# Kernel tuning notes

Hardware: AMD Instinct MI355X
Metric: run time of the kernel (lower is better)

The kernel has to match this reference:

```python
import jax, jax.numpy as jnp
import numpy as np

GAMMA = 0.1
B, C, H, W = 8, 64, 64, 64
CINT = C // 8


def setup_inputs() -> dict:
    key = jax.random.key(0)
    ks = jax.random.split(key, 5)
    x = jax.random.normal(ks[0], (B, C, H, W), dtype=jnp.float32)
    Wq = jax.random.normal(ks[1], (CINT, C), dtype=jnp.float32) * 0.05
    Wk = jax.random.normal(ks[2], (CINT, C), dtype=jnp.float32) * 0.05
    Wv = jax.random.normal(ks[3], (CINT, C), dtype=jnp.float32) * 0.05
    Wout = jax.random.normal(ks[4], (C, CINT), dtype=jnp.float32) * 0.05
    return {"x": x, "Wq": Wq, "Wk": Wk, "Wv": Wv, "Wout": Wout}


def reference(x, Wq, Wk, Wv, Wout):
    b, c, h, w = x.shape
    n = h * w
    cint = Wq.shape[0]
    xf = x.reshape(b, c, n)                               # [B,C,N]
    q = jnp.einsum('ic,bcn->bin', Wq, xf)                 # [B,Cint,N]
    k = jnp.einsum('ic,bcn->bin', Wk, xf)
    v = jnp.einsum('ic,bcn->bin', Wv, xf)
    # scores[b, n, m] = q[b,:,n] . k[b,:,m]; softmax over dim=1 (the n axis)
    scores = jnp.einsum('bin,bim->bnm', q, k) / jnp.sqrt(jnp.asarray(cint, x.dtype))
    att = jax.nn.softmax(scores, axis=1)                  # [B,N,N], softmax over rows
    att_out = jnp.einsum('bin,bnm->bim', v, att)          # [B,Cint,N]
    out = jnp.einsum('ci,bim->bcm', Wout, att_out)        # [B,C,N]
    return x + out.reshape(b, c, h, w) * GAMMA
```

## Files before the change

### kernel.cpp

```cpp
#include <hip/hip_runtime.h>
#include <math.h>

#define BB 8
#define CC 64
#define NN 4096
#define CI 8
#define GAMMA 0.1f
#define SCALE (1.44269504088896f * 0.35355339059327f)
#define NSPLIT 8

typedef float v4f  __attribute__((ext_vector_type(4)));
typedef float v16f __attribute__((ext_vector_type(16)));
typedef __bf16 bf16x8 __attribute__((ext_vector_type(8)));
typedef __bf16 bf16x4 __attribute__((ext_vector_type(4)));
typedef unsigned int u32x2 __attribute__((ext_vector_type(2)));

__device__ __forceinline__ float fast_exp2(float x) {
    return __builtin_amdgcn_exp2f(x);
}

__device__ __forceinline__ unsigned int cvt_pk_bf16(float lo, float hi) {
    unsigned int r;
    asm("v_cvt_pk_bf16_f32 %0, %1, %2" : "=v"(r) : "v"(lo), "v"(hi));
    return r;
}

__global__ __launch_bounds__(256) void qkv_kernel(
        const float* __restrict__ x,
        const float* __restrict__ Wq, const float* __restrict__ Wk,
        const float* __restrict__ Wv,
        __bf16* __restrict__ qbh, __bf16* __restrict__ kbh,
        __bf16* __restrict__ vbh, float* __restrict__ attab) {
    __shared__ float sw[3 * CI * CC];
    __shared__ unsigned short sq[32 * 8];
    __shared__ unsigned short sk[32 * 8];
    const int t = threadIdx.x;
    const int i  = t >> 5;
    const int nl = t & 31;
    const int b  = blockIdx.y;
    const int n0 = blockIdx.x * 32;

    for (int idx = t; idx < CI * CC; idx += 256) {
        sw[idx]                = Wq[idx];
        sw[CI * CC + idx]      = Wk[idx] * SCALE;
        sw[2 * CI * CC + idx]  = Wv[idx];
    }
    int lin = (blockIdx.y * (NN / 32) + blockIdx.x) * 256 + t;
    for (int idx = lin; idx < BB * 9 * NN; idx += BB * NN * CI) attab[idx] = 0.f;
    __syncthreads();

    const int n = n0 + nl;
    const float* xp = x + ((size_t)b * CC) * NN + n;
    const v4f* wq4 = (const v4f*)(sw + i * CC);
    const v4f* wk4 = (const v4f*)(sw + CI * CC + i * CC);
    const v4f* wv4 = (const v4f*)(sw + 2 * CI * CC + i * CC);
    float qa = 0.f, ka = 0.f, va = 0.f;
#pragma unroll 4
    for (int c4 = 0; c4 < CC / 4; ++c4) {
        v4f wq = wq4[c4], wk = wk4[c4], wv = wv4[c4];
        float x0 = xp[(size_t)(c4 * 4 + 0) * NN];
        float x1 = xp[(size_t)(c4 * 4 + 1) * NN];
        float x2 = xp[(size_t)(c4 * 4 + 2) * NN];
        float x3 = xp[(size_t)(c4 * 4 + 3) * NN];
        qa = fmaf(wq.x, x0, qa); ka = fmaf(wk.x, x0, ka); va = fmaf(wv.x, x0, va);
        qa = fmaf(wq.y, x1, qa); ka = fmaf(wk.y, x1, ka); va = fmaf(wv.y, x1, va);
        qa = fmaf(wq.z, x2, qa); ka = fmaf(wk.z, x2, ka); va = fmaf(wv.z, x2, va);
        qa = fmaf(wq.w, x3, qa); ka = fmaf(wk.w, x3, ka); va = fmaf(wv.w, x3, va);
    }
    __bf16 vb = (__bf16)va;
    vbh[((size_t)b * CI + i) * NN + n] = vb;
    __bf16 qb = (__bf16)qa, kb2 = (__bf16)ka;
    sq[nl * 8 + i] = *(unsigned short*)&qb;
    sk[nl * 8 + i] = *(unsigned short*)&kb2;
    __syncthreads();
    if (t < 32) {
        *(uint4*)(qbh + ((size_t)b * NN + n0 + t) * 8) = *(const uint4*)(sq + t * 8);
        *(uint4*)(kbh + ((size_t)b * NN + n0 + t) * 8) = *(const uint4*)(sk + t * 8);
    }
}

__global__ __launch_bounds__(256) void att_kernel(
        const __bf16* __restrict__ qbh, const __bf16* __restrict__ kbh,
        const __bf16* __restrict__ vbh, float* __restrict__ attab) {
    const int t = threadIdx.x;
    const int w    = t >> 6;
    const int l    = t & 63;
    const int ln   = l & 31;
    const int hi   = l >> 5;
    const int b  = blockIdx.z;
    const int m0 = blockIdx.x * 128 + w * 32;
    const int nbase = blockIdx.y * (NN / NSPLIT);
    const int NCH = (NN / NSPLIT) / 32;

    bf16x8 zero8, ones8;
#pragma unroll
    for (int z = 0; z < 8; ++z) { zero8[z] = (__bf16)0.0f; ones8[z] = (__bf16)1.0f; }

    bf16x8 kfragB = hi ? zero8
                       : *(const bf16x8*)(kbh + ((size_t)b * NN + m0 + ln) * 8);

    const __bf16* qrow = qbh + (size_t)b * NN * 8;
    const __bf16* vrow = vbh + ((size_t)b * CI + (ln & 7)) * NN;
    const bool v_live = (ln < 8);
    const bool v_ones = (ln == 8);

    v16f acc = {0.f,0.f,0.f,0.f,0.f,0.f,0.f,0.f,0.f,0.f,0.f,0.f,0.f,0.f,0.f,0.f};

    for (int ch = 0; ch < NCH; ++ch) {
        const int nc = nbase + ch * 32;
        bf16x8 qfrag = hi ? zero8
                          : *(const bf16x8*)(qrow + (size_t)(nc + ln) * 8);
        bf16x8 va0 = v_live ? *(const bf16x8*)(vrow + nc + hi * 8)
                            : (v_ones ? ones8 : zero8);
        bf16x8 va1 = v_live ? *(const bf16x8*)(vrow + nc + 16 + hi * 8)
                            : (v_ones ? ones8 : zero8);

        v16f S = __builtin_amdgcn_mfma_f32_32x32x16_bf16(
            qfrag, kfragB,
            (v16f){0.f,0.f,0.f,0.f,0.f,0.f,0.f,0.f,0.f,0.f,0.f,0.f,0.f,0.f,0.f,0.f},
            0, 0, 0);

        unsigned int pk0 = cvt_pk_bf16(fast_exp2(S[0]),  fast_exp2(S[1]));
        unsigned int pk1 = cvt_pk_bf16(fast_exp2(S[2]),  fast_exp2(S[3]));
        unsigned int pk2 = cvt_pk_bf16(fast_exp2(S[4]),  fast_exp2(S[5]));
        unsigned int pk3 = cvt_pk_bf16(fast_exp2(S[6]),  fast_exp2(S[7]));
        unsigned int pk4 = cvt_pk_bf16(fast_exp2(S[8]),  fast_exp2(S[9]));
        unsigned int pk5 = cvt_pk_bf16(fast_exp2(S[10]), fast_exp2(S[11]));
        unsigned int pk6 = cvt_pk_bf16(fast_exp2(S[12]), fast_exp2(S[13]));
        unsigned int pk7 = cvt_pk_bf16(fast_exp2(S[14]), fast_exp2(S[15]));

        u32x2 r02 = __builtin_amdgcn_permlane32_swap(pk0, pk2, false, false);
        u32x2 r13 = __builtin_amdgcn_permlane32_swap(pk1, pk3, false, false);
        u32x2 r46 = __builtin_amdgcn_permlane32_swap(pk4, pk6, false, false);
        u32x2 r57 = __builtin_amdgcn_permlane32_swap(pk5, pk7, false, false);

        union { unsigned int u[4]; bf16x8 f; } e0f, e1f;
        e0f.u[0] = r02[0]; e0f.u[1] = r13[0]; e0f.u[2] = r02[1]; e0f.u[3] = r13[1];
        e1f.u[0] = r46[0]; e1f.u[1] = r57[0]; e1f.u[2] = r46[1]; e1f.u[3] = r57[1];

        acc = __builtin_amdgcn_mfma_f32_32x32x16_bf16(va0, e0f.f, acc, 0, 0, 0);
        acc = __builtin_amdgcn_mfma_f32_32x32x16_bf16(va1, e1f.f, acc, 0, 0, 0);
    }

    float* ap = attab + (size_t)b * 9 * NN + m0 + ln;
#pragma unroll
    for (int r = 0; r < 16; ++r) {
        int io = (r & 3) + 8 * (r >> 2) + 4 * hi;
        if (io < 9) atomicAdd(ap + (size_t)io * NN, acc[r]);
    }
}

__global__ __launch_bounds__(256) void out_kernel(
        const float* __restrict__ x, const float* __restrict__ Wout,
        const float* __restrict__ attab, float* __restrict__ out) {
    const int t = threadIdx.x;
    const int c = blockIdx.y;
    const int b = blockIdx.z;
    const int m = (blockIdx.x * 256 + t) * 4;
    const float* ap = attab + (size_t)b * 9 * NN + m;
    v4f sum = *(const v4f*)(ap + (size_t)8 * NN);
    v4f s = {0.f, 0.f, 0.f, 0.f};
#pragma unroll
    for (int i = 0; i < CI; ++i) {
        float wgt = Wout[c * CI + i];
        v4f a = *(const v4f*)(ap + (size_t)i * NN);
        s.x = fmaf(wgt, a.x, s.x);
        s.y = fmaf(wgt, a.y, s.y);
        s.z = fmaf(wgt, a.z, s.z);
        s.w = fmaf(wgt, a.w, s.w);
    }
    size_t o = ((size_t)b * CC + c) * NN + m;
    v4f xv = *(const v4f*)(x + o);
    v4f r;
    r.x = xv.x + GAMMA * (s.x / sum.x);
    r.y = xv.y + GAMMA * (s.y / sum.y);
    r.z = xv.z + GAMMA * (s.z / sum.z);
    r.w = xv.w + GAMMA * (s.w / sum.w);
    *(v4f*)(out + o) = r;
}

extern "C" void kernel_launch(void* const* d_in, const int* in_sizes, int n_in,
                              void* d_out, int out_size, void* d_ws, size_t ws_size,
                              hipStream_t stream) {
    const float* x    = (const float*)d_in[0];
    const float* Wq   = (const float*)d_in[1];
    const float* Wk   = (const float*)d_in[2];
    const float* Wv   = (const float*)d_in[3];
    const float* Wout = (const float*)d_in[4];
    float* out = (float*)d_out;

    __bf16* qbh = (__bf16*)d_ws;
    __bf16* kbh = qbh + (size_t)BB * NN * 8;
    __bf16* vbh = kbh + (size_t)BB * NN * 8;
    float* attab = (float*)(vbh + (size_t)BB * NN * 8);

    qkv_kernel<<<dim3(NN / 32, BB), 256, 0, stream>>>(x, Wq, Wk, Wv, qbh, kbh, vbh, attab);
    att_kernel<<<dim3(NN / 128, NSPLIT, BB), 256, 0, stream>>>(qbh, kbh, vbh, attab);
    out_kernel<<<dim3(NN / 1024, CC, BB), 256, 0, stream>>>(x, Wout, attab, out);
}
```

Measured before the change: 108.3 us.

## Pad V to 32 rows, prefetch next chunk, split MFMA accumulators

V is stored as a 32-row padded buffer per batch, with a ones row and zero rows written by the qkv kernel. This removes the per-lane selects that previously built the ones and zero fragments in the attention loop. The attention loop now software-prefetches the next chunk's q and v fragments and alternates between two accumulators, which breaks the serial MFMA dependency chain. The cost is a four-times larger V buffer and extra global loads of constant padding rows.

```diff
diff --git a/kernel.cpp b/kernel.cpp
--- a/kernel.cpp
+++ b/kernel.cpp
@@ -30,7 +30,7 @@
         const float* __restrict__ Wq, const float* __restrict__ Wk,
         const float* __restrict__ Wv,
         __bf16* __restrict__ qbh, __bf16* __restrict__ kbh,
-        __bf16* __restrict__ vbh, float* __restrict__ attab) {
+        __bf16* __restrict__ vt, float* __restrict__ attab) {
     __shared__ float sw[3 * CI * CC];
     __shared__ unsigned short sq[32 * 8];
     __shared__ unsigned short sk[32 * 8];
@@ -47,6 +47,12 @@
     }
     int lin = (blockIdx.y * (NN / 32) + blockIdx.x) * 256 + t;
     for (int idx = lin; idx < BB * 9 * NN; idx += BB * NN * CI) attab[idx] = 0.f;
+    {
+        const __bf16 one = (__bf16)1.0f, zer = (__bf16)0.0f;
+        const int n = n0 + (t & 31);
+        for (int r = 8 + (t >> 5); r < 32; r += 8)
+            vt[((size_t)b * 32 + r) * NN + n] = (r == 8) ? one : zer;
+    }
     __syncthreads();
 
     const int n = n0 + nl;
@@ -68,7 +74,7 @@
         qa = fmaf(wq.w, x3, qa); ka = fmaf(wk.w, x3, ka); va = fmaf(wv.w, x3, va);
     }
     __bf16 vb = (__bf16)va;
-    vbh[((size_t)b * CI + i) * NN + n] = vb;
+    vt[((size_t)b * 32 + i) * NN + n] = vb;
     __bf16 qb = (__bf16)qa, kb2 = (__bf16)ka;
     sq[nl * 8 + i] = *(unsigned short*)&qb;
     sk[nl * 8 + i] = *(unsigned short*)&kb2;
@@ -81,7 +87,7 @@
 
 __global__ __launch_bounds__(256) void att_kernel(
         const __bf16* __restrict__ qbh, const __bf16* __restrict__ kbh,
-        const __bf16* __restrict__ vbh, float* __restrict__ attab) {
+        const __bf16* __restrict__ vt, float* __restrict__ attab) {
     const int t = threadIdx.x;
     const int w    = t >> 6;
     const int l    = t & 63;
@@ -92,33 +98,33 @@
     const int nbase = blockIdx.y * (NN / NSPLIT);
     const int NCH = (NN / NSPLIT) / 32;
 
-    bf16x8 zero8, ones8;
+    bf16x8 zero8;
 #pragma unroll
-    for (int z = 0; z < 8; ++z) { zero8[z] = (__bf16)0.0f; ones8[z] = (__bf16)1.0f; }
+    for (int z = 0; z < 8; ++z) zero8[z] = (__bf16)0.0f;
+    const v16f vzero = {0.f,0.f,0.f,0.f,0.f,0.f,0.f,0.f,
+                        0.f,0.f,0.f,0.f,0.f,0.f,0.f,0.f};
 
     bf16x8 kfragB = hi ? zero8
                        : *(const bf16x8*)(kbh + ((size_t)b * NN + m0 + ln) * 8);
 
     const __bf16* qrow = qbh + (size_t)b * NN * 8;
-    const __bf16* vrow = vbh + ((size_t)b * CI + (ln & 7)) * NN;
-    const bool v_live = (ln < 8);
-    const bool v_ones = (ln == 8);
-
-    v16f acc = {0.f,0.f,0.f,0.f,0.f,0.f,0.f,0.f,0.f,0.f,0.f,0.f,0.f,0.f,0.f,0.f};
-
+    const __bf16* vrow = vt + ((size_t)b * 32 + ln) * NN;
+
+    v16f acc0 = vzero, acc1 = vzero;
+
+    bf16x8 qf  = *(const bf16x8*)(qrow + (size_t)(nbase + ln) * 8);
+    bf16x8 va0 = *(const bf16x8*)(vrow + nbase + hi * 8);
+    bf16x8 va1 = *(const bf16x8*)(vrow + nbase + 16 + hi * 8);
+
+#pragma unroll 2
     for (int ch = 0; ch < NCH; ++ch) {
-        const int nc = nbase + ch * 32;
-        bf16x8 qfrag = hi ? zero8
-                          : *(const bf16x8*)(qrow + (size_t)(nc + ln) * 8);
-        bf16x8 va0 = v_live ? *(const bf16x8*)(vrow + nc + hi * 8)
-                            : (v_ones ? ones8 : zero8);
-        bf16x8 va1 = v_live ? *(const bf16x8*)(vrow + nc + 16 + hi * 8)
-                            : (v_ones ? ones8 : zero8);
-
-        v16f S = __builtin_amdgcn_mfma_f32_32x32x16_bf16(
-            qfrag, kfragB,
-            (v16f){0.f,0.f,0.f,0.f,0.f,0.f,0.f,0.f,0.f,0.f,0.f,0.f,0.f,0.f,0.f,0.f},
-            0, 0, 0);
+        const int ncn = nbase + ((ch + 1) & (NCH - 1)) * 32;
+        bf16x8 qf_n  = *(const bf16x8*)(qrow + (size_t)(ncn + ln) * 8);
+        bf16x8 va0_n = *(const bf16x8*)(vrow + ncn + hi * 8);
+        bf16x8 va1_n = *(const bf16x8*)(vrow + ncn + 16 + hi * 8);
+
+        v16f S = __builtin_amdgcn_mfma_f32_32x32x16_bf16(qf, kfragB, vzero,
+                                                         0, 0, 0);
 
         unsigned int pk0 = cvt_pk_bf16(fast_exp2(S[0]),  fast_exp2(S[1]));
         unsigned int pk1 = cvt_pk_bf16(fast_exp2(S[2]),  fast_exp2(S[3]));
@@ -138,15 +144,22 @@
         e0f.u[0] = r02[0]; e0f.u[1] = r13[0]; e0f.u[2] = r02[1]; e0f.u[3] = r13[1];
         e1f.u[0] = r46[0]; e1f.u[1] = r57[0]; e1f.u[2] = r46[1]; e1f.u[3] = r57[1];
 
-        acc = __builtin_amdgcn_mfma_f32_32x32x16_bf16(va0, e0f.f, acc, 0, 0, 0);
-        acc = __builtin_amdgcn_mfma_f32_32x32x16_bf16(va1, e1f.f, acc, 0, 0, 0);
+        if (ch & 1) {
+            acc1 = __builtin_amdgcn_mfma_f32_32x32x16_bf16(va0, e0f.f, acc1, 0, 0, 0);
+            acc1 = __builtin_amdgcn_mfma_f32_32x32x16_bf16(va1, e1f.f, acc1, 0, 0, 0);
+        } else {
+            acc0 = __builtin_amdgcn_mfma_f32_32x32x16_bf16(va0, e0f.f, acc0, 0, 0, 0);
+            acc0 = __builtin_amdgcn_mfma_f32_32x32x16_bf16(va1, e1f.f, acc0, 0, 0, 0);
+        }
+
+        qf = qf_n; va0 = va0_n; va1 = va1_n;
     }
 
     float* ap = attab + (size_t)b * 9 * NN + m0 + ln;
 #pragma unroll
     for (int r = 0; r < 16; ++r) {
         int io = (r & 3) + 8 * (r >> 2) + 4 * hi;
-        if (io < 9) atomicAdd(ap + (size_t)io * NN, acc[r]);
+        if (io < 9) atomicAdd(ap + (size_t)io * NN, acc0[r] + acc1[r]);
     }
 }
 
@@ -191,10 +204,10 @@
 
     __bf16* qbh = (__bf16*)d_ws;
     __bf16* kbh = qbh + (size_t)BB * NN * 8;
-    __bf16* vbh = kbh + (size_t)BB * NN * 8;
-    float* attab = (float*)(vbh + (size_t)BB * NN * 8);
-
-    qkv_kernel<<<dim3(NN / 32, BB), 256, 0, stream>>>(x, Wq, Wk, Wv, qbh, kbh, vbh, attab);
-    att_kernel<<<dim3(NN / 128, NSPLIT, BB), 256, 0, stream>>>(qbh, kbh, vbh, attab);
+    __bf16* vt  = kbh + (size_t)BB * NN * 8;
+    float* attab = (float*)(vt + (size_t)BB * NN * 32);
+
+    qkv_kernel<<<dim3(NN / 32, BB), 256, 0, stream>>>(x, Wq, Wk, Wv, qbh, kbh, vt, attab);
+    att_kernel<<<dim3(NN / 128, NSPLIT, BB), 256, 0, stream>>>(qbh, kbh, vt, attab);
     out_kernel<<<dim3(NN / 1024, CC, BB), 256, 0, stream>>>(x, Wout, attab, out);
 }
```

Result: slower. 114.5 us (+5.7%).

## Compute softmax denominator via VALU sums, drop masked loads, raise split

Applied to the files above, without the earlier changes.

The attention kernel no longer builds a ones-row inside the V operand to get the softmax column sums from the MFMA. Instead it sums the exponentials in registers per lane, combines the two half-waves with a shuffle, and issues one atomic per column. This removes the conditional V/Q loads and most of the per-element atomics. It also raises the N split from 8 to 16 for more parallelism and wraps the MFMAs in s_setprio. The trade-off is extra VALU adds per chunk and twice as many partial atomics into the accumulator buffer. Lanes with ln>=8 or hi=1 now load real Q and V data that the MFMA result never uses, so the results should stay correct.

```diff
diff --git a/kernel.cpp b/kernel.cpp
--- a/kernel.cpp
+++ b/kernel.cpp
@@ -7,12 +7,11 @@
 #define CI 8
 #define GAMMA 0.1f
 #define SCALE (1.44269504088896f * 0.35355339059327f)
-#define NSPLIT 8
+#define NSPLIT 16
 
 typedef float v4f  __attribute__((ext_vector_type(4)));
 typedef float v16f __attribute__((ext_vector_type(16)));
 typedef __bf16 bf16x8 __attribute__((ext_vector_type(8)));
-typedef __bf16 bf16x4 __attribute__((ext_vector_type(4)));
 typedef unsigned int u32x2 __attribute__((ext_vector_type(2)));
 
 __device__ __forceinline__ float fast_exp2(float x) {
@@ -92,42 +91,52 @@
     const int nbase = blockIdx.y * (NN / NSPLIT);
     const int NCH = (NN / NSPLIT) / 32;
 
-    bf16x8 zero8, ones8;
+    bf16x8 zero8;
 #pragma unroll
-    for (int z = 0; z < 8; ++z) { zero8[z] = (__bf16)0.0f; ones8[z] = (__bf16)1.0f; }
+    for (int z = 0; z < 8; ++z) zero8[z] = (__bf16)0.0f;
+    const v16f vzero = {0.f,0.f,0.f,0.f,0.f,0.f,0.f,0.f,
+                        0.f,0.f,0.f,0.f,0.f,0.f,0.f,0.f};
 
     bf16x8 kfragB = hi ? zero8
                        : *(const bf16x8*)(kbh + ((size_t)b * NN + m0 + ln) * 8);
 
     const __bf16* qrow = qbh + (size_t)b * NN * 8;
     const __bf16* vrow = vbh + ((size_t)b * CI + (ln & 7)) * NN;
-    const bool v_live = (ln < 8);
-    const bool v_ones = (ln == 8);
-
-    v16f acc = {0.f,0.f,0.f,0.f,0.f,0.f,0.f,0.f,0.f,0.f,0.f,0.f,0.f,0.f,0.f,0.f};
+
+    v16f acc = vzero;
+    float den = 0.f;
 
     for (int ch = 0; ch < NCH; ++ch) {
         const int nc = nbase + ch * 32;
-        bf16x8 qfrag = hi ? zero8
-                          : *(const bf16x8*)(qrow + (size_t)(nc + ln) * 8);
-        bf16x8 va0 = v_live ? *(const bf16x8*)(vrow + nc + hi * 8)
-                            : (v_ones ? ones8 : zero8);
-        bf16x8 va1 = v_live ? *(const bf16x8*)(vrow + nc + 16 + hi * 8)
-                            : (v_ones ? ones8 : zero8);
-
-        v16f S = __builtin_amdgcn_mfma_f32_32x32x16_bf16(
-            qfrag, kfragB,
-            (v16f){0.f,0.f,0.f,0.f,0.f,0.f,0.f,0.f,0.f,0.f,0.f,0.f,0.f,0.f,0.f,0.f},
-            0, 0, 0);
-
-        unsigned int pk0 = cvt_pk_bf16(fast_exp2(S[0]),  fast_exp2(S[1]));
-        unsigned int pk1 = cvt_pk_bf16(fast_exp2(S[2]),  fast_exp2(S[3]));
-        unsigned int pk2 = cvt_pk_bf16(fast_exp2(S[4]),  fast_exp2(S[5]));
-        unsigned int pk3 = cvt_pk_bf16(fast_exp2(S[6]),  fast_exp2(S[7]));
-        unsigned int pk4 = cvt_pk_bf16(fast_exp2(S[8]),  fast_exp2(S[9]));
-        unsigned int pk5 = cvt_pk_bf16(fast_exp2(S[10]), fast_exp2(S[11]));
-        unsigned int pk6 = cvt_pk_bf16(fast_exp2(S[12]), fast_exp2(S[13]));
-        unsigned int pk7 = cvt_pk_bf16(fast_exp2(S[14]), fast_exp2(S[15]));
+        bf16x8 qf  = *(const bf16x8*)(qrow + (size_t)(nc + ln) * 8);
+        bf16x8 va0 = *(const bf16x8*)(vrow + nc + hi * 8);
+        bf16x8 va1 = *(const bf16x8*)(vrow + nc + 16 + hi * 8);
+
+        __builtin_amdgcn_s_setprio(1);
+        v16f S = __builtin_amdgcn_mfma_f32_32x32x16_bf16(qf, kfragB, vzero,
+                                                         0, 0, 0);
+        __builtin_amdgcn_s_setprio(0);
+
+        float e0  = fast_exp2(S[0]),  e1  = fast_exp2(S[1]);
+        float e2  = fast_exp2(S[2]),  e3  = fast_exp2(S[3]);
+        float e4  = fast_exp2(S[4]),  e5  = fast_exp2(S[5]);
+        float e6  = fast_exp2(S[6]),  e7  = fast_exp2(S[7]);
+        float e8  = fast_exp2(S[8]),  e9  = fast_exp2(S[9]);
+        float e10 = fast_exp2(S[10]), e11 = fast_exp2(S[11]);
+        float e12 = fast_exp2(S[12]), e13 = fast_exp2(S[13]);
+        float e14 = fast_exp2(S[14]), e15 = fast_exp2(S[15]);
+
+        den += (((e0 + e1) + (e2 + e3)) + ((e4 + e5) + (e6 + e7)))
+             + (((e8 + e9) + (e10 + e11)) + ((e12 + e13) + (e14 + e15)));
+
+        unsigned int pk0 = cvt_pk_bf16(e0,  e1);
+        unsigned int pk1 = cvt_pk_bf16(e2,  e3);
+        unsigned int pk2 = cvt_pk_bf16(e4,  e5);
+        unsigned int pk3 = cvt_pk_bf16(e6,  e7);
+        unsigned int pk4 = cvt_pk_bf16(e8,  e9);
+        unsigned int pk5 = cvt_pk_bf16(e10, e11);
+        unsigned int pk6 = cvt_pk_bf16(e12, e13);
+        unsigned int pk7 = cvt_pk_bf16(e14, e15);
 
         u32x2 r02 = __builtin_amdgcn_permlane32_swap(pk0, pk2, false, false);
         u32x2 r13 = __builtin_amdgcn_permlane32_swap(pk1, pk3, false, false);
@@ -138,16 +147,19 @@
         e0f.u[0] = r02[0]; e0f.u[1] = r13[0]; e0f.u[2] = r02[1]; e0f.u[3] = r13[1];
         e1f.u[0] = r46[0]; e1f.u[1] = r57[0]; e1f.u[2] = r46[1]; e1f.u[3] = r57[1];
 
+        __builtin_amdgcn_s_setprio(1);
         acc = __builtin_amdgcn_mfma_f32_32x32x16_bf16(va0, e0f.f, acc, 0, 0, 0);
         acc = __builtin_amdgcn_mfma_f32_32x32x16_bf16(va1, e1f.f, acc, 0, 0, 0);
+        __builtin_amdgcn_s_setprio(0);
     }
 
     float* ap = attab + (size_t)b * 9 * NN + m0 + ln;
 #pragma unroll
-    for (int r = 0; r < 16; ++r) {
-        int io = (r & 3) + 8 * (r >> 2) + 4 * hi;
-        if (io < 9) atomicAdd(ap + (size_t)io * NN, acc[r]);
-    }
+    for (int r = 0; r < 4; ++r)
+        atomicAdd(ap + (size_t)(r + 4 * hi) * NN, acc[r]);
+    float dtot = den + __shfl_xor(den, 32, 64);
+    if (hi == 0)
+        atomicAdd(ap + (size_t)8 * NN, dtot);
 }
 
 __global__ __launch_bounds__(256) void out_kernel(
```

After: 120.5 us. +11.3%, slower.
